# Performance work log

Measured on AMD Instinct MI355X. Metric: run time of the kernel, lower is better.

The kernel has to match this reference:

```python
import jax, jax.numpy as jnp
import numpy as np

K = 4        # kernel_size
PAD = 2      # padding
GROUPS = 1   # groups


def _unfold(x, H, W):
    # x: [B, C, Hp, Wp] padded map; stride-1 KxK windows, sliced to first HxW
    # positions (matches torch unfold(2,K,1).unfold(3,K,1)[:, :, :H, :W]).
    # Returns [B, C, H, W, K*K].
    return jnp.stack([x[:, :, i:i + H, j:j + W]
                      for i in range(K) for j in range(K)], axis=-1)


def setup_inputs() -> dict:
    key = jax.random.key(0)
    ks = jax.random.split(key, 7)
    B, Cin, H, W, Cout = 8, 3, 128, 128, 64
    c = Cout // GROUPS
    return {
        "x": jax.random.normal(ks[0], (B, Cin, H, W), jnp.float32),
        "q_w": jax.random.normal(ks[1], (Cout, Cin), jnp.float32) * 0.2,
        "k_w": jax.random.normal(ks[2], (Cout, Cin), jnp.float32) * 0.2,
        "v_w": jax.random.normal(ks[3], (Cout, Cin), jnp.float32) * 0.2,
        "emb_a": jax.random.normal(ks[4], (c, W), jnp.float32),
        "emb_b": jax.random.normal(ks[5], (c, H), jnp.float32),
        "emb_mix": jax.random.normal(ks[6], (c, H, W), jnp.float32),
    }


def reference(x, q_w, k_w, v_w, emb_a, emb_b, emb_mix):
    B, Cin, H, W = x.shape
    O = q_w.shape[0]
    G = GROUPS
    c = O // G
    KK = K * K

    # 1x1 convs (no bias) as channel contractions
    q = jnp.einsum('oc,bchw->bohw', q_w, x)                      # [B,O,H,W]
    xp = jnp.pad(x, ((0, 0), (0, 0), (PAD, PAD), (PAD, PAD)))
    k = jnp.einsum('oc,bchw->bohw', k_w, xp)                     # [B,O,Hp,Wp]
    v = jnp.einsum('oc,bchw->bohw', v_w, xp)

    # im2col-style local windows -> [B,G,c,H,W,KK]
    k = _unfold(k, H, W).reshape(B, G, c, H, W, KK)
    v = _unfold(v, H, W).reshape(B, G, c, H, W, KK)

    # positional embedding logits (elementwise scale of v per (c,h,w))
    logit_a = v * emb_a[None, None, :, None, :, None]            # 'bnchwk,cw'
    logit_b = v * emb_b[None, None, :, :, None, None]            # 'bnchwk,ch'
    logit_mix = v * emb_mix[None, None, :, :, :, None]           # 'bnchwk,chw'
    embedding = jax.nn.softmax((logit_a + logit_b) * logit_mix, axis=-1)

    qr = q.reshape(B, G, c, H, W, 1)
    att = jax.nn.softmax(qr * k * embedding, axis=-1)            # double softmax
    out = jnp.sum(att * v, axis=-1).reshape(B, O, H, W)
    return out
```

## Files before the change

### kernel.cpp

```cpp
#include <hip/hip_runtime.h>

typedef float f4 __attribute__((ext_vector_type(4)));

static __device__ __forceinline__ f4 vmax4(f4 a, f4 b) {
  f4 r;
  r.x = fmaxf(a.x, b.x); r.y = fmaxf(a.y, b.y);
  r.z = fmaxf(a.z, b.z); r.w = fmaxf(a.w, b.w);
  return r;
}
static __device__ __forceinline__ f4 vexp2(f4 a) {
  f4 r;
  r.x = __builtin_amdgcn_exp2f(a.x); r.y = __builtin_amdgcn_exp2f(a.y);
  r.z = __builtin_amdgcn_exp2f(a.z); r.w = __builtin_amdgcn_exp2f(a.w);
  return r;
}
static __device__ __forceinline__ float hsum(f4 v) {
  return (v.x + v.y) + (v.z + v.w);
}

__global__ __launch_bounds__(256, 4) void stem_kernel(
    const float* __restrict__ x,
    const float* __restrict__ qwp,
    const float* __restrict__ kwp,
    const float* __restrict__ vwp,
    const float* __restrict__ ea,
    const float* __restrict__ eb,
    const float* __restrict__ em,
    float* __restrict__ out)
{
  __shared__ float xt[3][132][4];

  const int blk = blockIdx.x;
  const int b = blk >> 7;
  const int h = blk & 127;
  const int t = threadIdx.x;

  for (int idx = t; idx < 3 * 4 * 132; idx += 256) {
    int wp  = idx % 132;
    int rem = idx / 132;
    int rr  = rem & 3;
    int cin = rem >> 2;
    int sr = h - 2 + rr;
    int sc = wp - 2;
    float val = 0.0f;
    if ((unsigned)sr < 128u && (unsigned)sc < 128u)
      val = x[((b * 3 + cin) * 128 + sr) * 128 + sc];
    xt[cin][wp][rr] = val;
  }
  __syncthreads();

  const int w  = t & 127;
  const int cg = t >> 7;
  const float LOG2E = 1.4426950408889634f;

  f4 xw0[4], xw1[4], xw2[4];
#pragma unroll
  for (int j = 0; j < 4; ++j) {
    xw0[j] = *(const f4*)(&xt[0][w + j][0]);
    xw1[j] = *(const f4*)(&xt[1][w + j][0]);
    xw2[j] = *(const f4*)(&xt[2][w + j][0]);
  }

  const int base_c = cg * 32;
#pragma unroll 1
  for (int i = 0; i < 32; ++i) {
    const int c = __builtin_amdgcn_readfirstlane(base_c + i);

    const float kwa = kwp[c * 3 + 0], kwb = kwp[c * 3 + 1], kwc = kwp[c * 3 + 2];
    const float vwa = vwp[c * 3 + 0], vwb = vwp[c * 3 + 1], vwc = vwp[c * 3 + 2];
    const float qwa = qwp[c * 3 + 0], qwb = qwp[c * 3 + 1], qwc = qwp[c * 3 + 2];

    f4 kk[4], vv[4];
#pragma unroll
    for (int j = 0; j < 4; ++j) {
      kk[j] = kwa * xw0[j] + kwb * xw1[j] + kwc * xw2[j];
      vv[j] = vwa * xw0[j] + vwb * xw1[j] + vwc * xw2[j];
    }
    const float q = qwa * xw0[2].z + qwb * xw1[2].z + qwc * xw2[2].z;

    const float sp =
        (ea[c * 128 + w] + eb[c * 128 + h]) * em[(c * 128 + h) * 128 + w] * LOG2E;

    f4 tl[4];
#pragma unroll
    for (int j = 0; j < 4; ++j) tl[j] = (sp * vv[j]) * vv[j];

    f4 mm = vmax4(vmax4(tl[0], tl[1]), vmax4(tl[2], tl[3]));
    const float tmax = fmaxf(fmaxf(mm.x, mm.y), fmaxf(mm.z, mm.w));

    f4 e[4];
#pragma unroll
    for (int j = 0; j < 4; ++j) e[j] = vexp2(tl[j] - tmax);

    const float sum_e = hsum((e[0] + e[1]) + (e[2] + e[3]));
    const float qs = q * LOG2E * __builtin_amdgcn_rcpf(sum_e);

    f4 p[4];
#pragma unroll
    for (int j = 0; j < 4; ++j) p[j] = vexp2((qs * kk[j]) * e[j]);

    f4 ps4 = (p[0] + p[1]) + (p[2] + p[3]);
    f4 pv4 = p[0] * vv[0] + p[1] * vv[1];
    pv4 = pv4 + (p[2] * vv[2] + p[3] * vv[3]);

    const float denom = hsum(ps4);
    const float numer = hsum(pv4);

    out[((b * 64 + c) * 128 + h) * 128 + w] =
        numer * __builtin_amdgcn_rcpf(denom);
  }
}

extern "C" void kernel_launch(void* const* d_in, const int* in_sizes, int n_in,
                              void* d_out, int out_size, void* d_ws, size_t ws_size,
                              hipStream_t stream) {
  const float* x  = (const float*)d_in[0];
  const float* qw = (const float*)d_in[1];
  const float* kw = (const float*)d_in[2];
  const float* vw = (const float*)d_in[3];
  const float* ea = (const float*)d_in[4];
  const float* eb = (const float*)d_in[5];
  const float* em = (const float*)d_in[6];
  float* out = (float*)d_out;

  stem_kernel<<<dim3(8 * 128), dim3(256), 0, stream>>>(x, qw, kw, vw, ea, eb, em, out);
}
```

Baseline: 62.34 us.

## Tile blocks over 16 rows and 2 channels with sliding-window K/V reuse

The old kernel ran one block per (batch, row), with each thread looping over 32 channels. The new kernel runs one block per (batch, 16-row tile, channel pair). Each thread keeps its channel weights and embedding values in registers and walks down the rows, computing only one new K/V row per step and reusing the other three through a rotating register window. This cuts the redundant 1x1-conv recompute across the 4x4 window and the repeated weight loads, and it raises the block count from 1024 to 2048. In exchange each block stages a 19-row halo, so x is loaded about 1.2x, and the loop relies on register-component indexing that the compiler must resolve statically.

```diff
diff --git a/kernel.cpp b/kernel.cpp
--- a/kernel.cpp
+++ b/kernel.cpp
@@ -2,21 +2,24 @@
 
 typedef float f4 __attribute__((ext_vector_type(4)));
 
-static __device__ __forceinline__ f4 vmax4(f4 a, f4 b) {
+static __device__ __forceinline__ f4 vexp2(f4 a) {
+  f4 r;
+  r.x = __builtin_amdgcn_exp2f(a.x);
+  r.y = __builtin_amdgcn_exp2f(a.y);
+  r.z = __builtin_amdgcn_exp2f(a.z);
+  r.w = __builtin_amdgcn_exp2f(a.w);
+  return r;
+}
+static __device__ __forceinline__ f4 fmax4(f4 a, f4 b) {
   f4 r;
   r.x = fmaxf(a.x, b.x); r.y = fmaxf(a.y, b.y);
   r.z = fmaxf(a.z, b.z); r.w = fmaxf(a.w, b.w);
   return r;
 }
-static __device__ __forceinline__ f4 vexp2(f4 a) {
-  f4 r;
-  r.x = __builtin_amdgcn_exp2f(a.x); r.y = __builtin_amdgcn_exp2f(a.y);
-  r.z = __builtin_amdgcn_exp2f(a.z); r.w = __builtin_amdgcn_exp2f(a.w);
-  return r;
-}
-static __device__ __forceinline__ float hsum(f4 v) {
-  return (v.x + v.y) + (v.z + v.w);
-}
+
+#define LOG2E 1.4426950408889634f
+#define TILE 16
+#define ROWS (TILE + 3)
 
 __global__ __launch_bounds__(256, 4) void stem_kernel(
     const float* __restrict__ x,
@@ -28,87 +31,119 @@
     const float* __restrict__ em,
     float* __restrict__ out)
 {
-  __shared__ float xt[3][132][4];
+  __shared__ float xs[3][ROWS][132];
 
   const int blk = blockIdx.x;
-  const int b = blk >> 7;
-  const int h = blk & 127;
-  const int t = threadIdx.x;
+  const int cp = blk & 31;
+  const int ht = (blk >> 5) & 7;
+  const int b  = blk >> 8;
+  const int h0 = ht * TILE;
+  const int t  = threadIdx.x;
 
-  for (int idx = t; idx < 3 * 4 * 132; idx += 256) {
-    int wp  = idx % 132;
-    int rem = idx / 132;
-    int rr  = rem & 3;
-    int cin = rem >> 2;
-    int sr = h - 2 + rr;
-    int sc = wp - 2;
-    float val = 0.0f;
-    if ((unsigned)sr < 128u && (unsigned)sc < 128u)
-      val = x[((b * 3 + cin) * 128 + sr) * 128 + sc];
-    xt[cin][wp][rr] = val;
+  {
+    const float* xb = x + b * (3 * 128 * 128);
+    for (int idx = t; idx < 3 * ROWS * 128; idx += 256) {
+      int row = idx >> 7;
+      int wp2 = idx & 127;
+      int cin = (row >= ROWS) + (row >= 2 * ROWS);
+      int rr  = row - cin * ROWS;
+      int g   = h0 - 2 + rr;
+      float v = 0.f;
+      if ((unsigned)g < 128u) v = xb[(cin * 128 + g) * 128 + wp2];
+      xs[cin][rr][wp2 + 2] = v;
+    }
+    if (t < 3 * ROWS * 4) {
+      int row = t >> 2;
+      int col = t & 3;
+      int wp  = (col & 1) + ((col >> 1) ? 130 : 0);
+      int cin = (row >= ROWS) + (row >= 2 * ROWS);
+      int rr  = row - cin * ROWS;
+      xs[cin][rr][wp] = 0.f;
+    }
   }
   __syncthreads();
 
   const int w  = t & 127;
   const int cg = t >> 7;
-  const float LOG2E = 1.4426950408889634f;
+  const int c  = __builtin_amdgcn_readfirstlane(cp * 2 + cg);
 
-  f4 xw0[4], xw1[4], xw2[4];
+  const float kwa = kwp[c * 3], kwb = kwp[c * 3 + 1], kwc = kwp[c * 3 + 2];
+  const float vwa = vwp[c * 3], vwb = vwp[c * 3 + 1], vwc = vwp[c * 3 + 2];
+  const float qwa = qwp[c * 3], qwb = qwp[c * 3 + 1], qwc = qwp[c * 3 + 2];
+
+  const float ea_c = ea[c * 128 + w];
+  const float* ebp = eb + c * 128 + h0;
+  const float* emp = em + (c * 128 + h0) * 128 + w;
+  float* outp = out + ((b * 64 + c) * 128 + h0) * 128 + w;
+
+  f4 kk[4], vv[4];
+
+#define SLIDE(RR, COMP)                                        \
+  do {                                                         \
+    _Pragma("unroll")                                          \
+    for (int j = 0; j < 4; ++j) {                              \
+      float x0 = xs[0][RR][w + j];                             \
+      float x1 = xs[1][RR][w + j];                             \
+      float x2 = xs[2][RR][w + j];                             \
+      kk[j][COMP] = kwc * x2 + (kwa * x0 + kwb * x1);          \
+      vv[j][COMP] = vwc * x2 + (vwa * x0 + vwb * x1);          \
+    }                                                          \
+  } while (0)
+
+  SLIDE(0, 0);
+  SLIDE(1, 1);
+  SLIDE(2, 2);
+
+  float em_cur = emp[0];
+
+#pragma unroll 1
+  for (int s4 = 0; s4 < TILE / 4; ++s4) {
 #pragma unroll
-  for (int j = 0; j < 4; ++j) {
-    xw0[j] = *(const f4*)(&xt[0][w + j][0]);
-    xw1[j] = *(const f4*)(&xt[1][w + j][0]);
-    xw2[j] = *(const f4*)(&xt[2][w + j][0]);
+    for (int phi = 0; phi < 4; ++phi) {
+      const int s = s4 * 4 + phi;
+      SLIDE(s + 3, ((phi + 3) & 3));
+
+      const float em_nxt = emp[(s + 1 < TILE ? s + 1 : s) * 128];
+      const float eb_s = ebp[s];
+
+      const float q = qwa * xs[0][s + 2][w + 2] + qwb * xs[1][s + 2][w + 2] +
+                      qwc * xs[2][s + 2][w + 2];
+
+      const float sp = (ea_c + eb_s) * em_cur * LOG2E;
+
+      f4 e0 = (sp * vv[0]) * vv[0];
+      f4 e1 = (sp * vv[1]) * vv[1];
+      f4 e2 = (sp * vv[2]) * vv[2];
+      f4 e3 = (sp * vv[3]) * vv[3];
+
+      f4 mm = fmax4(fmax4(e0, e1), fmax4(e2, e3));
+      const float tmax = fmaxf(fmaxf(mm.x, mm.y), fmaxf(mm.z, mm.w));
+
+      e0 = vexp2(e0 - tmax);
+      e1 = vexp2(e1 - tmax);
+      e2 = vexp2(e2 - tmax);
+      e3 = vexp2(e3 - tmax);
+
+      f4 se = (e0 + e1) + (e2 + e3);
+      const float sum_e = (se.x + se.y) + (se.z + se.w);
+      const float qs = q * LOG2E * __builtin_amdgcn_rcpf(sum_e);
+
+      f4 p0 = vexp2((qs * kk[0]) * e0);
+      f4 p1 = vexp2((qs * kk[1]) * e1);
+      f4 p2 = vexp2((qs * kk[2]) * e2);
+      f4 p3 = vexp2((qs * kk[3]) * e3);
+
+      f4 ps = (p0 + p1) + (p2 + p3);
+      f4 pv = (p0 * vv[0] + p1 * vv[1]) + (p2 * vv[2] + p3 * vv[3]);
+
+      const float denom = (ps.x + ps.y) + (ps.z + ps.w);
+      const float numer = (pv.x + pv.y) + (pv.z + pv.w);
+
+      outp[s * 128] = numer * __builtin_amdgcn_rcpf(denom);
+      em_cur = em_nxt;
+    }
   }
-
-  const int base_c = cg * 32;
-#pragma unroll 1
-  for (int i = 0; i < 32; ++i) {
-    const int c = __builtin_amdgcn_readfirstlane(base_c + i);
-
-    const float kwa = kwp[c * 3 + 0], kwb = kwp[c * 3 + 1], kwc = kwp[c * 3 + 2];
-    const float vwa = vwp[c * 3 + 0], vwb = vwp[c * 3 + 1], vwc = vwp[c * 3 + 2];
-    const float qwa = qwp[c * 3 + 0], qwb = qwp[c * 3 + 1], qwc = qwp[c * 3 + 2];
-
-    f4 kk[4], vv[4];
-#pragma unroll
-    for (int j = 0; j < 4; ++j) {
-      kk[j] = kwa * xw0[j] + kwb * xw1[j] + kwc * xw2[j];
-      vv[j] = vwa * xw0[j] + vwb * xw1[j] + vwc * xw2[j];
-    }
-    const float q = qwa * xw0[2].z + qwb * xw1[2].z + qwc * xw2[2].z;
-
-    const float sp =
-        (ea[c * 128 + w] + eb[c * 128 + h]) * em[(c * 128 + h) * 128 + w] * LOG2E;
-
-    f4 tl[4];
-#pragma unroll
-    for (int j = 0; j < 4; ++j) tl[j] = (sp * vv[j]) * vv[j];
-
-    f4 mm = vmax4(vmax4(tl[0], tl[1]), vmax4(tl[2], tl[3]));
-    const float tmax = fmaxf(fmaxf(mm.x, mm.y), fmaxf(mm.z, mm.w));
-
-    f4 e[4];
-#pragma unroll
-    for (int j = 0; j < 4; ++j) e[j] = vexp2(tl[j] - tmax);
-
-    const float sum_e = hsum((e[0] + e[1]) + (e[2] + e[3]));
-    const float qs = q * LOG2E * __builtin_amdgcn_rcpf(sum_e);
-
-    f4 p[4];
-#pragma unroll
-    for (int j = 0; j < 4; ++j) p[j] = vexp2((qs * kk[j]) * e[j]);
-
-    f4 ps4 = (p[0] + p[1]) + (p[2] + p[3]);
-    f4 pv4 = p[0] * vv[0] + p[1] * vv[1];
-    pv4 = pv4 + (p[2] * vv[2] + p[3] * vv[3]);
-
-    const float denom = hsum(ps4);
-    const float numer = hsum(pv4);
-
-    out[((b * 64 + c) * 128 + h) * 128 + w] =
-        numer * __builtin_amdgcn_rcpf(denom);
-  }
+#undef SLIDE
 }
 
 extern "C" void kernel_launch(void* const* d_in, const int* in_sizes, int n_in,
@@ -123,5 +158,5 @@
   const float* em = (const float*)d_in[6];
   float* out = (float*)d_out;
 
-  stem_kernel<<<dim3(8 * 128), dim3(256), 0, stream>>>(x, qw, kw, vw, ea, eb, em, out);
+  stem_kernel<<<dim3(8 * 8 * 32), dim3(256), 0, stream>>>(x, qw, kw, vw, ea, eb, em, out);
 }
```

Result: slower. 227.7 us (+265.2%).
